# Optimization experiments

Measured on AMD Instinct MI355X. Metric: run time of the kernel, lower is better.

The kernel has to match this reference:

```python
import jax, jax.numpy as jnp
import numpy as np

B, H, LQ, LK, D, HID = 2, 1, 512, 512, 64, 128


def setup_inputs() -> dict:
    key = jax.random.key(0)
    ks = jax.random.split(key, 8)
    f = lambda k, shape, s=1.0: jax.random.normal(k, shape, dtype=jnp.float32) * s
    return {
        "q": f(ks[0], (B, H, LQ, D)),
        "k": f(ks[1], (B, H, LK, D)),
        "v": f(ks[2], (B, H, LK, D)),
        "mask": jnp.zeros((B, H, LQ, LK), jnp.float32),
        # shared q/k/v projection (self.w) and output projection (self.dense)
        "Ww": f(ks[3], (D, D), 0.1), "wb": jnp.zeros((D,), jnp.float32),
        "Wd": f(ks[4], (D, D), 0.1), "db": jnp.zeros((D,), jnp.float32),
        # two-layer MLP NN: 2*D -> HID -> 1
        "W1": f(ks[5], (2 * D, HID), 0.1), "b1": jnp.zeros((HID,), jnp.float32),
        "W2": f(ks[6], (HID, 1), 0.1), "b2": jnp.zeros((1,), jnp.float32),
    }


def _sim_scores(q, k, W1, b1, W2, b2, make_sym):
    # Equivalent to tile+concat+MLP, but splits W1 so the 2*D concat tensor
    # is never materialized; only the [B,H,Lq,Lk,HID] hidden is.
    W1q, W1k = W1[:D], W1[D:]
    qa = q @ W1q  # [B,H,Lq,HID]
    kb = k @ W1k  # [B,H,Lk,HID]
    h = jax.nn.relu(qa[:, :, :, None, :] + kb[:, :, None, :, :] + b1)
    s = (h @ W2)[..., 0] + b2[0]  # [B,H,Lq,Lk]
    if make_sym:
        # concat([k, q]) order: hidden2 = relu(k_j @ W1q + q_i @ W1k + b1)
        qb = q @ W1k
        ka = k @ W1q
        h2 = jax.nn.relu(qb[:, :, :, None, :] + ka[:, :, None, :, :] + b1)
        s = s + (h2 @ W2)[..., 0] + b2[0]
    return s


def reference(q, k, v, mask, Ww, wb, Wd, db, W1, b1, W2, b2):
    make_sym = True
    qp = q @ Ww + wb
    kp = k @ Ww + wb
    vp = v @ Ww + wb
    logits = _sim_scores(qp, kp, W1, b1, W2, b2, make_sym)
    logits = logits + mask * (-1e9)
    attn = jax.nn.softmax(logits, axis=-1)  # [B,H,Lq,Lk]
    out = attn @ vp                          # [B,H,Lq,D]
    out = out @ Wd + db
    return (out, attn)
```

## Files before the change

### kernel.cpp

```cpp
#include <hip/hip_runtime.h>
#include <hip/hip_bf16.h>


#define NROWS 1024
#define DD    64
#define HH    128
#define LK_   512
#define QR    4

__global__ __launch_bounds__(128)
void proj_kernel(const float* __restrict__ q, const float* __restrict__ k,
                 const float* __restrict__ v,
                 const float* __restrict__ Ww, const float* __restrict__ wb,
                 const float* __restrict__ W1, const float* __restrict__ b1,
                 float* __restrict__ qp, float* __restrict__ kp, float* __restrict__ vp,
                 float* __restrict__ qa, float* __restrict__ qb,
                 float* __restrict__ ka, float* __restrict__ kb)
{
    const int r    = blockIdx.x;
    const int type = r >> 10;
    const int idx  = r & 1023;
    const int t    = threadIdx.x;

    const float* src = (type == 0) ? q : (type == 1) ? k : v;

    __shared__ float x[DD];
    __shared__ float xp[DD];

    if (t < DD) x[t] = src[idx * DD + t];
    __syncthreads();

    if (t < DD) {
        float acc = wb[t];
        #pragma unroll
        for (int c = 0; c < DD; ++c) acc = fmaf(x[c], Ww[c * DD + t], acc);
        xp[t] = acc;
        float* dst = (type == 0) ? qp : (type == 1) ? kp : vp;
        dst[idx * DD + t] = acc;
    }
    __syncthreads();

    if (type == 2) return;

    float accA = 0.f;
    float accB = 0.f;
    #pragma unroll
    for (int d = 0; d < DD; ++d) {
        const float xv = xp[d];
        accA = fmaf(xv, W1[d * HH + t],        accA);
        accB = fmaf(xv, W1[(DD + d) * HH + t], accB);
    }
    if (type == 0) {
        qa[idx * HH + t] = accA + b1[t];
        qb[idx * HH + t] = accB + b1[t];
    } else {
        ka[idx * HH + t] = accA;
        kb[idx * HH + t] = accB;
    }
}

__global__ __launch_bounds__(512)
void attn_kernel(const float* __restrict__ mask,
                 const float* __restrict__ vp,
                 const float* __restrict__ qa, const float* __restrict__ qb,
                 const float* __restrict__ ka, const float* __restrict__ kb,
                 const float* __restrict__ W2, const float* __restrict__ b2,
                 const float* __restrict__ Wd, const float* __restrict__ db,
                 float* __restrict__ out, float* __restrict__ attn)
{
    const int row0 = blockIdx.x * QR;
    const int b    = row0 >> 9;
    const int t    = threadIdx.x;
    const int wid  = t >> 6;
    const int lane = t & 63;

    __shared__ float qa_l[QR][HH];
    __shared__ float qb_l[QR][HH];
    __shared__ float w2_l[HH];
    __shared__ float p[QR][LK_];
    __shared__ float redm[8][QR];
    __shared__ float reds[8][QR];
    __shared__ float opart[8][QR][DD];
    __shared__ float o_l[QR][DD];

    if (t < QR * HH) {
        const int r = t >> 7, h = t & (HH - 1);
        qa_l[r][h] = qa[(row0 + r) * HH + h];
        qb_l[r][h] = qb[(row0 + r) * HH + h];
    }
    if (t < HH) w2_l[t] = W2[t];
    __syncthreads();

    const float b2v = b2[0];
    const int   j    = t;
    const int   jrow = b * LK_ + j;
    const float4* kbr = reinterpret_cast<const float4*>(kb + jrow * HH);
    const float4* kar = reinterpret_cast<const float4*>(ka + jrow * HH);

    float s1[QR] = {0.f, 0.f, 0.f, 0.f};
    float s2[QR] = {0.f, 0.f, 0.f, 0.f};
    #pragma unroll 4
    for (int h4 = 0; h4 < HH / 4; ++h4) {
        const float4 kb4 = kbr[h4];
        const float4 ka4 = kar[h4];
        const int h = h4 * 4;
        const float w0 = w2_l[h + 0], w1 = w2_l[h + 1];
        const float w2v = w2_l[h + 2], w3 = w2_l[h + 3];
        #pragma unroll
        for (int r = 0; r < QR; ++r) {
            s1[r] = fmaf(fmaxf(qa_l[r][h + 0] + kb4.x, 0.f), w0, s1[r]);
            s1[r] = fmaf(fmaxf(qa_l[r][h + 1] + kb4.y, 0.f), w1, s1[r]);
            s1[r] = fmaf(fmaxf(qa_l[r][h + 2] + kb4.z, 0.f), w2v, s1[r]);
            s1[r] = fmaf(fmaxf(qa_l[r][h + 3] + kb4.w, 0.f), w3, s1[r]);
            s2[r] = fmaf(fmaxf(qb_l[r][h + 0] + ka4.x, 0.f), w0, s2[r]);
            s2[r] = fmaf(fmaxf(qb_l[r][h + 1] + ka4.y, 0.f), w1, s2[r]);
            s2[r] = fmaf(fmaxf(qb_l[r][h + 2] + ka4.z, 0.f), w2v, s2[r]);
            s2[r] = fmaf(fmaxf(qb_l[r][h + 3] + ka4.w, 0.f), w3, s2[r]);
        }
    }

    float sv[QR];
    #pragma unroll
    for (int r = 0; r < QR; ++r)
        sv[r] = s1[r] + s2[r] + 2.f * b2v + mask[(row0 + r) * LK_ + j] * (-1e9f);

    float m[QR];
    #pragma unroll
    for (int r = 0; r < QR; ++r) {
        float mv = sv[r];
        #pragma unroll
        for (int off = 32; off > 0; off >>= 1) mv = fmaxf(mv, __shfl_xor(mv, off));
        m[r] = mv;
        if (lane == 0) redm[wid][r] = mv;
    }
    __syncthreads();
    #pragma unroll
    for (int r = 0; r < QR; ++r) {
        float mv = redm[0][r];
        #pragma unroll
        for (int w = 1; w < 8; ++w) mv = fmaxf(mv, redm[w][r]);
        m[r] = mv;
    }

    float e[QR], sum[QR];
    #pragma unroll
    for (int r = 0; r < QR; ++r) {
        e[r] = expf(sv[r] - m[r]);
        float s = e[r];
        #pragma unroll
        for (int off = 32; off > 0; off >>= 1) s += __shfl_xor(s, off);
        if (lane == 0) reds[wid][r] = s;
    }
    __syncthreads();
    #pragma unroll
    for (int r = 0; r < QR; ++r) {
        float s = reds[0][r];
        #pragma unroll
        for (int w = 1; w < 8; ++w) s += reds[w][r];
        sum[r] = s;
    }

    #pragma unroll
    for (int r = 0; r < QR; ++r) {
        const float pv = e[r] / sum[r];
        p[r][j] = pv;
        attn[(row0 + r) * LK_ + j] = pv;
    }
    __syncthreads();

    float acc[QR] = {0.f, 0.f, 0.f, 0.f};
    {
        const int j0 = wid * 64;
        const float* vpb = vp + (b * LK_ + j0) * DD;
        #pragma unroll 8
        for (int jj = 0; jj < 64; ++jj) {
            const float vv = vpb[jj * DD + lane];
            #pragma unroll
            for (int r = 0; r < QR; ++r)
                acc[r] = fmaf(p[r][j0 + jj], vv, acc[r]);
        }
    }
    #pragma unroll
    for (int r = 0; r < QR; ++r) opart[wid][r][lane] = acc[r];
    __syncthreads();

    if (t < QR * DD) {
        const int r = t >> 6, d = t & 63;
        float o = opart[0][r][d];
        #pragma unroll
        for (int w = 1; w < 8; ++w) o += opart[w][r][d];
        o_l[r][d] = o;
    }
    __syncthreads();

    if (t < QR * DD) {
        const int r = t >> 6, d = t & 63;
        float res = db[d];
        #pragma unroll
        for (int c = 0; c < DD; ++c) res = fmaf(o_l[r][c], Wd[c * DD + d], res);
        out[(row0 + r) * DD + d] = res;
    }
}

extern "C" void kernel_launch(void* const* d_in, const int* in_sizes, int n_in,
                              void* d_out, int out_size, void* d_ws, size_t ws_size,
                              hipStream_t stream)
{
    const float* q    = (const float*)d_in[0];
    const float* k    = (const float*)d_in[1];
    const float* v    = (const float*)d_in[2];
    const float* mask = (const float*)d_in[3];
    const float* Ww   = (const float*)d_in[4];
    const float* wb   = (const float*)d_in[5];
    const float* Wd   = (const float*)d_in[6];
    const float* db   = (const float*)d_in[7];
    const float* W1   = (const float*)d_in[8];
    const float* b1   = (const float*)d_in[9];
    const float* W2   = (const float*)d_in[10];
    const float* b2   = (const float*)d_in[11];

    float* ws = (float*)d_ws;
    float* qp = ws;
    float* kp = qp + NROWS * DD;
    float* vp = kp + NROWS * DD;
    float* qa = vp + NROWS * DD;
    float* qb = qa + NROWS * HH;
    float* ka = qb + NROWS * HH;
    float* kb = ka + NROWS * HH;

    float* out  = (float*)d_out;
    float* attn = out + NROWS * DD;

    proj_kernel<<<dim3(3072), dim3(128), 0, stream>>>(
        q, k, v, Ww, wb, W1, b1, qp, kp, vp, qa, qb, ka, kb);

    attn_kernel<<<dim3(NROWS / QR), dim3(512), 0, stream>>>(
        mask, vp, qa, qb, ka, kb, W2, b2, Wd, db, out, attn);
}
```

Baseline: 107.6 us.

## Transpose ka/kb into interleaved h-major layout for coalesced attention loads

Adds a transpose kernel that rewrites ka and kb into an [B][H][LK] float2 interleaved layout, so each attention thread reads consecutive j values with coalesced loads instead of strided per-row float4 loads. The attention kernel also drops its LDS staging of qa/qb/W2 and reads those values directly from global memory, where they are uniform across threads. The cost is an extra kernel launch plus extra workspace traffic, and possibly less latency hiding now that the inner loop is unrolled per h instead of per 4 h.

Measured after the change: 106.6 us. About the same (-1.0%).

```diff
diff --git a/kernel.cpp b/kernel.cpp
--- a/kernel.cpp
+++ b/kernel.cpp
@@ -59,11 +59,39 @@
     }
 }
 
+__global__ __launch_bounds__(256)
+void trans_kernel(const float* __restrict__ ka, const float* __restrict__ kb,
+                  float2* __restrict__ kt)
+{
+    const int j0 = blockIdx.x * 64;
+    const int h0 = blockIdx.y * 64;
+    const int b  = blockIdx.z;
+    const int tx = threadIdx.x & 63;
+    const int ty = threadIdx.x >> 6;
+
+    __shared__ float ta[64][65];
+    __shared__ float tb[64][65];
+
+    #pragma unroll
+    for (int rr = 0; rr < 16; ++rr) {
+        const int jl = ty + rr * 4;
+        const int g  = (b * LK_ + j0 + jl) * HH + h0 + tx;
+        ta[jl][tx] = ka[g];
+        tb[jl][tx] = kb[g];
+    }
+    __syncthreads();
+    #pragma unroll
+    for (int rr = 0; rr < 16; ++rr) {
+        const int hl = ty + rr * 4;
+        kt[(b * HH + h0 + hl) * LK_ + j0 + tx] = make_float2(ta[tx][hl], tb[tx][hl]);
+    }
+}
+
 __global__ __launch_bounds__(512)
 void attn_kernel(const float* __restrict__ mask,
                  const float* __restrict__ vp,
                  const float* __restrict__ qa, const float* __restrict__ qb,
-                 const float* __restrict__ ka, const float* __restrict__ kb,
+                 const float2* __restrict__ kt,
                  const float* __restrict__ W2, const float* __restrict__ b2,
                  const float* __restrict__ Wd, const float* __restrict__ db,
                  float* __restrict__ out, float* __restrict__ attn)
@@ -73,52 +101,32 @@
     const int t    = threadIdx.x;
     const int wid  = t >> 6;
     const int lane = t & 63;
-
-    __shared__ float qa_l[QR][HH];
-    __shared__ float qb_l[QR][HH];
-    __shared__ float w2_l[HH];
+    const int j    = t;
+
     __shared__ float p[QR][LK_];
     __shared__ float redm[8][QR];
     __shared__ float reds[8][QR];
     __shared__ float opart[8][QR][DD];
     __shared__ float o_l[QR][DD];
 
-    if (t < QR * HH) {
-        const int r = t >> 7, h = t & (HH - 1);
-        qa_l[r][h] = qa[(row0 + r) * HH + h];
-        qb_l[r][h] = qb[(row0 + r) * HH + h];
-    }
-    if (t < HH) w2_l[t] = W2[t];
-    __syncthreads();
-
-    const float b2v = b2[0];
-    const int   j    = t;
-    const int   jrow = b * LK_ + j;
-    const float4* kbr = reinterpret_cast<const float4*>(kb + jrow * HH);
-    const float4* kar = reinterpret_cast<const float4*>(ka + jrow * HH);
+    const float2* ktb = kt + b * HH * LK_;
+    const float*  qaR = qa + row0 * HH;
+    const float*  qbR = qb + row0 * HH;
 
     float s1[QR] = {0.f, 0.f, 0.f, 0.f};
     float s2[QR] = {0.f, 0.f, 0.f, 0.f};
-    #pragma unroll 4
-    for (int h4 = 0; h4 < HH / 4; ++h4) {
-        const float4 kb4 = kbr[h4];
-        const float4 ka4 = kar[h4];
-        const int h = h4 * 4;
-        const float w0 = w2_l[h + 0], w1 = w2_l[h + 1];
-        const float w2v = w2_l[h + 2], w3 = w2_l[h + 3];
+    #pragma unroll 8
+    for (int h = 0; h < HH; ++h) {
+        const float2 kv = ktb[h * LK_ + j];
+        const float  w  = W2[h];
         #pragma unroll
         for (int r = 0; r < QR; ++r) {
-            s1[r] = fmaf(fmaxf(qa_l[r][h + 0] + kb4.x, 0.f), w0, s1[r]);
-            s1[r] = fmaf(fmaxf(qa_l[r][h + 1] + kb4.y, 0.f), w1, s1[r]);
-            s1[r] = fmaf(fmaxf(qa_l[r][h + 2] + kb4.z, 0.f), w2v, s1[r]);
-            s1[r] = fmaf(fmaxf(qa_l[r][h + 3] + kb4.w, 0.f), w3, s1[r]);
-            s2[r] = fmaf(fmaxf(qb_l[r][h + 0] + ka4.x, 0.f), w0, s2[r]);
-            s2[r] = fmaf(fmaxf(qb_l[r][h + 1] + ka4.y, 0.f), w1, s2[r]);
-            s2[r] = fmaf(fmaxf(qb_l[r][h + 2] + ka4.z, 0.f), w2v, s2[r]);
-            s2[r] = fmaf(fmaxf(qb_l[r][h + 3] + ka4.w, 0.f), w3, s2[r]);
+            s1[r] = fmaf(fmaxf(qaR[r * HH + h] + kv.y, 0.f), w, s1[r]);
+            s2[r] = fmaf(fmaxf(qbR[r * HH + h] + kv.x, 0.f), w, s2[r]);
         }
     }
 
+    const float b2v = b2[0];
     float sv[QR];
     #pragma unroll
     for (int r = 0; r < QR; ++r)
@@ -227,6 +235,7 @@
     float* qb = qa + NROWS * HH;
     float* ka = qb + NROWS * HH;
     float* kb = ka + NROWS * HH;
+    float2* kt = (float2*)(kb + NROWS * HH);
 
     float* out  = (float*)d_out;
     float* attn = out + NROWS * DD;
@@ -234,6 +243,8 @@
     proj_kernel<<<dim3(3072), dim3(128), 0, stream>>>(
         q, k, v, Ww, wb, W1, b1, qp, kp, vp, qa, qb, ka, kb);
 
+    trans_kernel<<<dim3(8, 2, 2), dim3(256), 0, stream>>>(ka, kb, kt);
+
     attn_kernel<<<dim3(NROWS / QR), dim3(512), 0, stream>>>(
-        mask, vp, qa, qb, ka, kb, W2, b2, Wd, db, out, attn);
-}
+        mask, vp, qa, qb, kt, W2, b2, Wd, db, out, attn);
+}
```
